# Kernel optimization log

Measured on AMD Instinct MI355X. Metric: run time of the kernel, lower is better.

Reference implementation:

```python
import jax, jax.numpy as jnp
import numpy as np

B, S, D, N = 8, 4096, 1024, 16
EPS = 1e-6


def setup_inputs() -> dict:
    key = jax.random.key(0)
    ks = jax.random.split(key, 6)
    s = 1.0 / np.sqrt(D)
    return {
        "x": jax.random.normal(ks[0], (B, S, D), dtype=jnp.float32),
        "W_lambda": jax.random.uniform(ks[1], (N, D), jnp.float32, -s, s),
        "b_lambda": jnp.full((N,), 2.0, dtype=jnp.float32),  # nn.init.constant_(bias, 2.0)
        "W_B": jax.random.uniform(ks[2], (N, D), jnp.float32, -s, s),
        "W_C": jax.random.uniform(ks[3], (D, N), jnp.float32, -1.0 / np.sqrt(N), 1.0 / np.sqrt(N)),
        "W_gate": jax.random.uniform(ks[4], (D, D), jnp.float32, -s, s),
        "rms_weight": jnp.ones((D,), dtype=jnp.float32),
    }


def reference(x, W_lambda, b_lambda, W_B, W_C, W_gate, rms_weight):
    # Input-dependent decay and input projection, computed for all timesteps at once
    lam = jax.nn.sigmoid(jnp.einsum("bsd,nd->bsn", x, W_lambda) + b_lambda)  # (B,S,N)
    Bx = jnp.einsum("bsd,nd->bsn", x, W_B)  # (B,S,N)

    def step(h, inp):
        l_t, b_t = inp
        h = l_t * h + b_t  # h_t = lambda_t * h_{t-1} + B_t x_t
        return h, h

    h0 = jnp.zeros((x.shape[0], W_B.shape[0]), dtype=x.dtype)
    _, hs = jax.lax.scan(step, h0, (jnp.swapaxes(lam, 0, 1), jnp.swapaxes(Bx, 0, 1)))
    hs = jnp.swapaxes(hs, 0, 1)  # (B,S,N)

    y = jnp.einsum("bsn,dn->bsd", hs, W_C)  # C @ h_t
    gate = jax.nn.sigmoid(jnp.einsum("bsd,ed->bse", x, W_gate))
    y = gate * y
    # RMSNorm
    rms = jax.lax.rsqrt(jnp.mean(y * y, axis=-1, keepdims=True) + EPS)
    return y * rms * rms_weight
```

## Files before the change

kernel.cpp:

```cpp
#include <hip/hip_runtime.h>

#define DD 1024
#define NN 16
#define SS 4096
#define BBATCH 8
#define TOK (BBATCH*SS)

typedef __attribute__((ext_vector_type(8))) __bf16 bf16x8;
typedef __attribute__((ext_vector_type(4))) __bf16 bf16x4;
typedef __attribute__((ext_vector_type(4))) float f32x4;
typedef unsigned int u32;
typedef unsigned long long u64;

__device__ __forceinline__ void async16(void* lds, const void* g) {
  __builtin_amdgcn_global_load_lds(
      (const __attribute__((address_space(1))) u32*)(u64)(g),
      (__attribute__((address_space(3))) u32*)(u32)(u64)(lds), 16, 0, 0);
}

__device__ __forceinline__ float sigmoidf_(float v) {
  return 1.f / (1.f + __expf(-v));
}

__global__ void k_cvtw(const float* __restrict__ wgf, const float* __restrict__ wlf,
                       const float* __restrict__ wbf, __bf16* __restrict__ wg,
                       __bf16* __restrict__ wp) {
  int i = blockIdx.x * blockDim.x + threadIdx.x;
  const int NG = DD * DD / 8, NP = NN * DD / 8;
  const float* src; __bf16* dst;
  if (i < NG)           { src = wgf + (u64)i * 8;            dst = wg + (u64)i * 8; }
  else if (i < NG + NP) { int j = i - NG; src = wlf + j * 8; dst = wp + j * 8; }
  else if (i < NG + 2 * NP) { int j = i - NG - NP; src = wbf + j * 8; dst = wp + NN * DD + j * 8; }
  else return;
  float4 a = *(const float4*)src, b = *(const float4*)(src + 4);
  bf16x8 o;
  o[0] = (__bf16)a.x; o[1] = (__bf16)a.y; o[2] = (__bf16)a.z; o[3] = (__bf16)a.w;
  o[4] = (__bf16)b.x; o[5] = (__bf16)b.y; o[6] = (__bf16)b.z; o[7] = (__bf16)b.w;
  *(bf16x8*)dst = o;
}

__global__ __launch_bounds__(256)
void k_proj(const float* __restrict__ x, const __bf16* __restrict__ wp,
            const float* __restrict__ b_lambda, __bf16* __restrict__ xb,
            float* __restrict__ lam, float* __restrict__ bx) {
  __shared__ __align__(16) __bf16 sA[128 * 32];
  __shared__ __align__(16) __bf16 sB[32 * 32];
  int tid = threadIdx.x;
  int lane = tid & 63, w = tid >> 6;
  int tok0 = blockIdx.x * 128;
  int crow = tid >> 1, cs = (tid & 1) * 2;
  const float* xsrc = x + (u64)(tok0 + crow) * DD + (tid & 1) * 16;
  __bf16* xdst = xb + (u64)(tok0 + crow) * DD + (tid & 1) * 16;
  int sw = (crow & 3) ^ ((crow >> 2) & 3);
  u64 bSrc;
  {
    int u = tid;
    int row = u >> 2, slot = (u & 3) ^ (row & 3);
    bSrc = (u64)((const char*)wp + ((u64)row * DD + slot * 8) * 2);
  }
  f32x4 acc[2][2] = {};
  int r15 = lane & 15, kg = lane >> 4;
  for (int kt = 0; kt < DD / 32; ++kt) {
    float4 a0 = *(const float4*)(xsrc + kt * 32 + 0);
    float4 a1 = *(const float4*)(xsrc + kt * 32 + 4);
    float4 a2 = *(const float4*)(xsrc + kt * 32 + 8);
    float4 a3 = *(const float4*)(xsrc + kt * 32 + 12);
    bf16x8 lo, hi;
    lo[0] = (__bf16)a0.x; lo[1] = (__bf16)a0.y; lo[2] = (__bf16)a0.z; lo[3] = (__bf16)a0.w;
    lo[4] = (__bf16)a1.x; lo[5] = (__bf16)a1.y; lo[6] = (__bf16)a1.z; lo[7] = (__bf16)a1.w;
    hi[0] = (__bf16)a2.x; hi[1] = (__bf16)a2.y; hi[2] = (__bf16)a2.z; hi[3] = (__bf16)a2.w;
    hi[4] = (__bf16)a3.x; hi[5] = (__bf16)a3.y; hi[6] = (__bf16)a3.z; hi[7] = (__bf16)a3.w;
    *(bf16x8*)(xdst + kt * 32) = lo;
    *(bf16x8*)(xdst + kt * 32 + 8) = hi;
    *(bf16x8*)((char*)sA + crow * 64 + ((cs ^ sw) << 4)) = lo;
    *(bf16x8*)((char*)sA + crow * 64 + (((cs + 1) ^ sw) << 4)) = hi;
    if (tid < 128)
      async16((char*)sB + w * 1024, (const void*)(bSrc + kt * 64));
    __syncthreads();
    bf16x8 bfr[2];
#pragma unroll
    for (int nt = 0; nt < 2; ++nt) {
      int brow = nt * 16 + r15;
      bfr[nt] = *(const bf16x8*)((const char*)sB + brow * 64 + ((kg ^ (brow & 3)) << 4));
    }
#pragma unroll
    for (int mt = 0; mt < 2; ++mt) {
      int arow = w * 32 + mt * 16 + r15;
      bf16x8 af = *(const bf16x8*)((const char*)sA + arow * 64 +
                                   ((kg ^ (arow & 3) ^ ((arow >> 2) & 3)) << 4));
#pragma unroll
      for (int nt = 0; nt < 2; ++nt)
        acc[mt][nt] = __builtin_amdgcn_mfma_f32_16x16x32_bf16(af, bfr[nt], acc[mt][nt], 0, 0, 0);
    }
    __syncthreads();
  }
#pragma unroll
  for (int mt = 0; mt < 2; ++mt)
#pragma unroll
    for (int nt = 0; nt < 2; ++nt)
#pragma unroll
      for (int r = 0; r < 4; ++r) {
        int token = tok0 + w * 32 + mt * 16 + kg * 4 + r;
        int j = nt * 16 + r15;
        float v = acc[mt][nt][r];
        if (j < 16) lam[token * NN + j] = sigmoidf_(v + b_lambda[j]);
        else        bx[token * NN + (j - 16)] = v;
      }
}

__global__ __launch_bounds__(256)
void k_scan(const float* __restrict__ lam, const float* __restrict__ bx,
            float* __restrict__ hs) {
  int b = blockIdx.x >> 4, n = blockIdx.x & 15;
  int t = threadIdx.x;
  const int CH = SS / 256;
  float lv[CH], bv[CH];
  int base = (b * SS + t * CH) * NN + n;
  float a = 1.f, bacc = 0.f;
#pragma unroll
  for (int i = 0; i < CH; ++i) {
    lv[i] = lam[base + i * NN];
    bv[i] = bx[base + i * NN];
    bacc = lv[i] * bacc + bv[i];
    a *= lv[i];
  }
  __shared__ float As[2][256], Bs[2][256];
  As[0][t] = a; Bs[0][t] = bacc;
  __syncthreads();
  int cur = 0;
  for (int off = 1; off < 256; off <<= 1) {
    float a2 = As[cur][t], b2 = Bs[cur][t];
    if (t >= off) {
      float ap = As[cur][t - off], bp = Bs[cur][t - off];
      b2 = b2 + a2 * bp;
      a2 = a2 * ap;
    }
    As[cur ^ 1][t] = a2; Bs[cur ^ 1][t] = b2;
    cur ^= 1;
    __syncthreads();
  }
  float h = (t == 0) ? 0.f : Bs[cur][t - 1];
#pragma unroll
  for (int i = 0; i < CH; ++i) {
    h = lv[i] * h + bv[i];
    hs[base + i * NN] = h;
  }
}

#define STG(kt, bi) do { u32 lb = (u32)(bi) * 32768u; u64 ko = (u64)(kt) * 64u;          \
    async16(smc + lb + (u32)w * 1024u,              (const void*)(aAddr0 + ko));         \
    async16(smc + lb + (u32)(8 + w) * 1024u,        (const void*)(aAddr1 + ko));         \
    async16(smc + lb + 16384u + (u32)w * 1024u,     (const void*)(bAddr0 + ko));         \
    async16(smc + lb + 16384u + (u32)(8 + w) * 1024u,(const void*)(bAddr1 + ko)); } while (0)

template<int YB16>
__global__ __launch_bounds__(512, 2)
void k_gemm(const __bf16* __restrict__ xb, const __bf16* __restrict__ wg,
            const float* __restrict__ hs, const float* __restrict__ wc,
            float* __restrict__ outf, __bf16* __restrict__ outb) {
  __shared__ __align__(16) char smc[131072];
  const int tid = threadIdx.x, lane = tid & 63, w = tid >> 6;
  const int r15 = lane & 15, kg = lane >> 4;
  const int wr = w >> 2, wcq = w & 3;
  int bid = blockIdx.x;
  int swz = (bid & 7) * 64 + (bid >> 3);
  int m = swz >> 2, n = swz & 3;
  const int tok0 = m * 256, n0 = n * 256;
  const int sslot = (lane & 3) ^ ((lane >> 2) & 3) ^ ((lane >> 4) & 3);
  const int rA0 = w * 16 + (lane >> 2);
  const int rA1 = (8 + w) * 16 + (lane >> 2);
  const u64 aAddr0 = (u64)(const char*)xb + (u64)(tok0 + rA0) * 2048 + (u32)sslot * 16;
  const u64 aAddr1 = (u64)(const char*)xb + (u64)(tok0 + rA1) * 2048 + (u32)sslot * 16;
  const u64 bAddr0 = (u64)(const char*)wg + (u64)(n0 + rA0) * 2048 + (u32)sslot * 16;
  const u64 bAddr1 = (u64)(const char*)wg + (u64)(n0 + rA1) * 2048 + (u32)sslot * 16;

  f32x4 acc[8][4] = {};

  STG(0, 0); STG(1, 1); STG(2, 2);
  asm volatile("s_waitcnt vmcnt(8)" ::: "memory");
  __builtin_amdgcn_s_barrier();
  __builtin_amdgcn_sched_barrier(0);

  for (int t = 0; t < 32; ++t) {
    if (t + 3 < 32) STG(t + 3, (t + 3) & 3);
    const char* Ab = smc + (t & 3) * 32768;
    const char* Bb = Ab + 16384;
    bf16x8 af[8];
#pragma unroll
    for (int mt = 0; mt < 8; ++mt) {
      int row = wr * 128 + mt * 16 + r15;
      int sl = kg ^ (row & 3) ^ ((row >> 2) & 3);
      af[mt] = *(const bf16x8*)(Ab + row * 64 + sl * 16);
    }
    __builtin_amdgcn_s_setprio(1);
#pragma unroll
    for (int nt = 0; nt < 4; ++nt) {
      int brow = wcq * 64 + nt * 16 + r15;
      int sl = kg ^ (brow & 3) ^ ((brow >> 2) & 3);
      bf16x8 bfr = *(const bf16x8*)(Bb + brow * 64 + sl * 16);
#pragma unroll
      for (int mt = 0; mt < 8; ++mt)
        acc[mt][nt] = __builtin_amdgcn_mfma_f32_16x16x32_bf16(af[mt], bfr, acc[mt][nt], 0, 0, 0);
    }
    __builtin_amdgcn_s_setprio(0);
    if (t < 29)       asm volatile("s_waitcnt vmcnt(8)" ::: "memory");
    else if (t == 29) asm volatile("s_waitcnt vmcnt(4)" ::: "memory");
    else              asm volatile("s_waitcnt vmcnt(0)" ::: "memory");
    __builtin_amdgcn_s_barrier();
    __builtin_amdgcn_sched_barrier(0);
  }

  float* hsl = (float*)smc;
  float* wcl = (float*)(smc + 20480);
  for (int idx = tid; idx < 256 * 16; idx += 512) {
    int r = idx >> 4, c = idx & 15;
    hsl[r * 20 + c] = hs[(u64)tok0 * NN + idx];
    wcl[r * 20 + c] = wc[(u64)n0 * NN + idx];
  }
  __syncthreads();
  f32x4 wcv[4][4];
#pragma unroll
  for (int nt = 0; nt < 4; ++nt) {
    int j = wcq * 64 + nt * 16 + r15;
#pragma unroll
    for (int q = 0; q < 4; ++q) wcv[nt][q] = *(const f32x4*)(wcl + j * 20 + q * 4);
  }
#pragma unroll
  for (int mt = 0; mt < 8; ++mt)
#pragma unroll
    for (int r = 0; r < 4; ++r) {
      int i = wr * 128 + mt * 16 + kg * 4 + r;
      f32x4 hv[4];
#pragma unroll
      for (int q = 0; q < 4; ++q) hv[q] = *(const f32x4*)(hsl + i * 20 + q * 4);
#pragma unroll
      for (int nt = 0; nt < 4; ++nt) {
        f32x4 cv = hv[0] * wcv[nt][0];
        cv += hv[1] * wcv[nt][1];
        cv += hv[2] * wcv[nt][2];
        cv += hv[3] * wcv[nt][3];
        float cy = cv[0] + cv[1] + cv[2] + cv[3];
        float g = sigmoidf_(acc[mt][nt][r]);
        int j = wcq * 64 + nt * 16 + r15;
        u64 off = (u64)(tok0 + i) * DD + n0 + j;
        if (YB16) outb[off] = (__bf16)(g * cy);
        else      outf[off] = g * cy;
      }
    }
}

__global__ __launch_bounds__(256)
void k_norm_b(const __bf16* __restrict__ yb, float* __restrict__ out,
              const float* __restrict__ rw) {
  int row = blockIdx.x * 4 + (threadIdx.x >> 6);
  int lane = threadIdx.x & 63;
  const __bf16* yrow = yb + (u64)row * DD;
  bf16x4 v[4];
  float f[16];
  float rs = 0.f;
#pragma unroll
  for (int q = 0; q < 4; ++q) {
    v[q] = *(const bf16x4*)(yrow + q * 256 + lane * 4);
#pragma unroll
    for (int e = 0; e < 4; ++e) {
      f[q * 4 + e] = (float)v[q][e];
      rs += f[q * 4 + e] * f[q * 4 + e];
    }
  }
#pragma unroll
  for (int msk = 1; msk < 64; msk <<= 1) rs += __shfl_xor(rs, msk, 64);
  float rstd = rsqrtf(rs * (1.f / DD) + 1e-6f);
  float* orow = out + (u64)row * DD;
#pragma unroll
  for (int q = 0; q < 4; ++q) {
    float4 wv = *(const float4*)(rw + q * 256 + lane * 4);
    float4 o;
    o.x = f[q * 4 + 0] * rstd * wv.x;
    o.y = f[q * 4 + 1] * rstd * wv.y;
    o.z = f[q * 4 + 2] * rstd * wv.z;
    o.w = f[q * 4 + 3] * rstd * wv.w;
    *(float4*)(orow + q * 256 + lane * 4) = o;
  }
}

__global__ __launch_bounds__(256)
void k_norm_f(float* __restrict__ out, const float* __restrict__ rw) {
  int row = blockIdx.x * 4 + (threadIdx.x >> 6);
  int lane = threadIdx.x & 63;
  float4* p = (float4*)(out + (u64)row * DD);
  float4 v[4];
  float rs = 0.f;
#pragma unroll
  for (int e = 0; e < 4; ++e) {
    v[e] = p[e * 64 + lane];
    rs += v[e].x * v[e].x + v[e].y * v[e].y + v[e].z * v[e].z + v[e].w * v[e].w;
  }
#pragma unroll
  for (int msk = 1; msk < 64; msk <<= 1) rs += __shfl_xor(rs, msk, 64);
  float rstd = rsqrtf(rs * (1.f / DD) + 1e-6f);
  const float4* rwp = (const float4*)rw;
#pragma unroll
  for (int e = 0; e < 4; ++e) {
    float4 wv = rwp[e * 64 + lane];
    float4 o;
    o.x = v[e].x * rstd * wv.x;
    o.y = v[e].y * rstd * wv.y;
    o.z = v[e].z * rstd * wv.z;
    o.w = v[e].w * rstd * wv.w;
    p[e * 64 + lane] = o;
  }
}

extern "C" void kernel_launch(void* const* d_in, const int* in_sizes, int n_in,
                              void* d_out, int out_size, void* d_ws, size_t ws_size,
                              hipStream_t stream) {
  (void)in_sizes; (void)n_in; (void)out_size;
  const float* x        = (const float*)d_in[0];
  const float* W_lambda = (const float*)d_in[1];
  const float* b_lambda = (const float*)d_in[2];
  const float* W_B      = (const float*)d_in[3];
  const float* W_C      = (const float*)d_in[4];
  const float* W_gate   = (const float*)d_in[5];
  const float* rms_w    = (const float*)d_in[6];
  char* ws = (char*)d_ws;
  __bf16* xb  = (__bf16*)(ws + 0);
  __bf16* wg  = (__bf16*)(ws + 67108864);
  __bf16* wp  = (__bf16*)(ws + 69206016);
  float*  lam = (float*)(ws + 69271552);
  float*  bx  = (float*)(ws + 71368704);
  float*  hs  = (float*)(ws + 73465856);
  __bf16* yb  = (__bf16*)(ws + 75563008);
  float*  out = (float*)d_out;
  bool yb16 = ws_size >= (size_t)(75563008ull + 67108864ull);

  k_cvtw<<<(DD * DD / 8 + 2 * NN * DD / 8 + 255) / 256, 256, 0, stream>>>(
      W_gate, W_lambda, W_B, wg, wp);
  k_proj<<<TOK / 128, 256, 0, stream>>>(x, wp, b_lambda, xb, lam, bx);
  k_scan<<<BBATCH * NN, 256, 0, stream>>>(lam, bx, hs);
  if (yb16) {
    k_gemm<1><<<(TOK / 256) * (DD / 256), 512, 0, stream>>>(xb, wg, hs, W_C, nullptr, yb);
    k_norm_b<<<TOK / 4, 256, 0, stream>>>(yb, out, rms_w);
  } else {
    k_gemm<0><<<(TOK / 256) * (DD / 256), 512, 0, stream>>>(xb, wg, hs, W_C, out, nullptr);
    k_norm_f<<<TOK / 4, 256, 0, stream>>>(out, rms_w);
  }
}
```

Measured before the change: 206.2 us.

## Restructure gate GEMM mainloop into 8-phase ping-pong with K=64 tiles

Replaces the 4-deep ring of K=32 tiles with a double-buffered scheme of K=64 tiles, each split into A/B halves of 128 rows. The loads for future tiles are interleaved between four MFMA phases, each fenced by barriers, and the LDS swizzle is changed to an 8-slot XOR pattern. The aim is to overlap global-to-LDS copies and LDS reads with MFMA work more finely and to halve the number of loop iterations. In exchange it adds many more barriers per iteration and depends on hand-tuned vmcnt and lgkmcnt waits being correct.

```diff
diff --git a/kernel.cpp b/kernel.cpp
--- a/kernel.cpp
+++ b/kernel.cpp
@@ -147,11 +147,12 @@
   }
 }
 
-#define STG(kt, bi) do { u32 lb = (u32)(bi) * 32768u; u64 ko = (u64)(kt) * 64u;          \
-    async16(smc + lb + (u32)w * 1024u,              (const void*)(aAddr0 + ko));         \
-    async16(smc + lb + (u32)(8 + w) * 1024u,        (const void*)(aAddr1 + ko));         \
-    async16(smc + lb + 16384u + (u32)w * 1024u,     (const void*)(bAddr0 + ko));         \
-    async16(smc + lb + 16384u + (u32)(8 + w) * 1024u,(const void*)(bAddr1 + ko)); } while (0)
+#define STAGE(tile, M, h) do {                                                    \
+    u32 lds0 = (u32)(((((tile) & 1) * 4 + (M) * 2 + (h)) << 14) + tid * 16);      \
+    u64 g0 = ((M) ? bBase : aBase) + ((u64)(h) << 18) + (u64)(tile) * 128;        \
+    async16(smc + lds0, (const void*)g0);                                         \
+    async16(smc + lds0 + 8192, (const void*)(g0 + 131072));                       \
+  } while (0)
 
 template<int YB16>
 __global__ __launch_bounds__(512, 2)
@@ -166,49 +167,111 @@
   int swz = (bid & 7) * 64 + (bid >> 3);
   int m = swz >> 2, n = swz & 3;
   const int tok0 = m * 256, n0 = n * 256;
-  const int sslot = (lane & 3) ^ ((lane >> 2) & 3) ^ ((lane >> 4) & 3);
-  const int rA0 = w * 16 + (lane >> 2);
-  const int rA1 = (8 + w) * 16 + (lane >> 2);
-  const u64 aAddr0 = (u64)(const char*)xb + (u64)(tok0 + rA0) * 2048 + (u32)sslot * 16;
-  const u64 aAddr1 = (u64)(const char*)xb + (u64)(tok0 + rA1) * 2048 + (u32)sslot * 16;
-  const u64 bAddr0 = (u64)(const char*)wg + (u64)(n0 + rA0) * 2048 + (u32)sslot * 16;
-  const u64 bAddr1 = (u64)(const char*)wg + (u64)(n0 + rA1) * 2048 + (u32)sslot * 16;
+  const int sslot = (tid & 7) ^ ((tid >> 3) & 7);
+  const u64 aBase = (u64)(const char*)xb + (u64)(tok0 + (tid >> 3)) * 2048 + (u32)sslot * 16;
+  const u64 bBase = (u64)(const char*)wg + (u64)(n0 + (tid >> 3)) * 2048 + (u32)sslot * 16;
+  const u32 sxa0 = (u32)(((0 | kg) ^ (r15 & 7)) * 16);
+  const u32 sxa1 = (u32)(((4 | kg) ^ (r15 & 7)) * 16);
+  const u32 lrB0 = (u32)((wcq & 1) * 64);
 
   f32x4 acc[8][4] = {};
 
-  STG(0, 0); STG(1, 1); STG(2, 2);
-  asm volatile("s_waitcnt vmcnt(8)" ::: "memory");
+  STAGE(0, 0, 0); STAGE(0, 0, 1); STAGE(0, 1, 0); STAGE(0, 1, 1);
+  STAGE(1, 1, 0); STAGE(1, 1, 1); STAGE(1, 0, 0);
+  asm volatile("s_waitcnt vmcnt(6)" ::: "memory");
   __builtin_amdgcn_s_barrier();
-  __builtin_amdgcn_sched_barrier(0);
-
-  for (int t = 0; t < 32; ++t) {
-    if (t + 3 < 32) STG(t + 3, (t + 3) & 3);
-    const char* Ab = smc + (t & 3) * 32768;
-    const char* Bb = Ab + 16384;
-    bf16x8 af[8];
-#pragma unroll
-    for (int mt = 0; mt < 8; ++mt) {
-      int row = wr * 128 + mt * 16 + r15;
-      int sl = kg ^ (row & 3) ^ ((row >> 2) & 3);
-      af[mt] = *(const bf16x8*)(Ab + row * 64 + sl * 16);
-    }
+  asm volatile("" ::: "memory");
+
+  for (int k = 0; k < 16; ++k) {
+    const int b = k & 1;
+    const char* Ah = smc + (u32)((b * 4 + wr) << 14);
+    const char* Bh = smc + (u32)((b * 4 + 2 + (wcq >> 1)) << 14);
+    bf16x8 af[8][2], bfr[4][2];
+#pragma unroll
+    for (int mt = 0; mt < 2; ++mt) {
+      u32 ro = (u32)(mt * 16 + r15) * 128;
+      af[mt][0] = *(const bf16x8*)(Ah + ro + sxa0);
+      af[mt][1] = *(const bf16x8*)(Ah + ro + sxa1);
+    }
+#pragma unroll
+    for (int nt = 0; nt < 4; ++nt) {
+      u32 ro = (lrB0 + (u32)(nt * 16 + r15)) * 128;
+      bfr[nt][0] = *(const bf16x8*)(Bh + ro + sxa0);
+      bfr[nt][1] = *(const bf16x8*)(Bh + ro + sxa1);
+    }
+    if (k <= 14) STAGE(k + 1, 0, 1);
+    __builtin_amdgcn_s_barrier();
+    asm volatile("s_waitcnt lgkmcnt(0)" ::: "memory");
+    __builtin_amdgcn_sched_barrier(0);
     __builtin_amdgcn_s_setprio(1);
 #pragma unroll
-    for (int nt = 0; nt < 4; ++nt) {
-      int brow = wcq * 64 + nt * 16 + r15;
-      int sl = kg ^ (brow & 3) ^ ((brow >> 2) & 3);
-      bf16x8 bfr = *(const bf16x8*)(Bb + brow * 64 + sl * 16);
-#pragma unroll
-      for (int mt = 0; mt < 8; ++mt)
-        acc[mt][nt] = __builtin_amdgcn_mfma_f32_16x16x32_bf16(af[mt], bfr, acc[mt][nt], 0, 0, 0);
-    }
+    for (int mt = 0; mt < 2; ++mt)
+#pragma unroll
+      for (int nt = 0; nt < 4; ++nt) {
+        acc[mt][nt] = __builtin_amdgcn_mfma_f32_16x16x32_bf16(af[mt][0], bfr[nt][0], acc[mt][nt], 0, 0, 0);
+        acc[mt][nt] = __builtin_amdgcn_mfma_f32_16x16x32_bf16(af[mt][1], bfr[nt][1], acc[mt][nt], 0, 0, 0);
+      }
     __builtin_amdgcn_s_setprio(0);
-    if (t < 29)       asm volatile("s_waitcnt vmcnt(8)" ::: "memory");
-    else if (t == 29) asm volatile("s_waitcnt vmcnt(4)" ::: "memory");
-    else              asm volatile("s_waitcnt vmcnt(0)" ::: "memory");
-    __builtin_amdgcn_s_barrier();
+    __builtin_amdgcn_s_barrier();
+    asm volatile("" ::: "memory");
+#pragma unroll
+    for (int mt = 2; mt < 6; ++mt) {
+      u32 ro = (u32)(mt * 16 + r15) * 128;
+      af[mt][0] = *(const bf16x8*)(Ah + ro + sxa0);
+      af[mt][1] = *(const bf16x8*)(Ah + ro + sxa1);
+    }
+    if (k <= 13) STAGE(k + 2, 1, 0);
+    __builtin_amdgcn_s_barrier();
+    asm volatile("s_waitcnt lgkmcnt(0)" ::: "memory");
     __builtin_amdgcn_sched_barrier(0);
-  }
+    __builtin_amdgcn_s_setprio(1);
+#pragma unroll
+    for (int mt = 2; mt < 4; ++mt)
+#pragma unroll
+      for (int nt = 0; nt < 4; ++nt) {
+        acc[mt][nt] = __builtin_amdgcn_mfma_f32_16x16x32_bf16(af[mt][0], bfr[nt][0], acc[mt][nt], 0, 0, 0);
+        acc[mt][nt] = __builtin_amdgcn_mfma_f32_16x16x32_bf16(af[mt][1], bfr[nt][1], acc[mt][nt], 0, 0, 0);
+      }
+    __builtin_amdgcn_s_setprio(0);
+    __builtin_amdgcn_s_barrier();
+    asm volatile("" ::: "memory");
+#pragma unroll
+    for (int mt = 6; mt < 8; ++mt) {
+      u32 ro = (u32)(mt * 16 + r15) * 128;
+      af[mt][0] = *(const bf16x8*)(Ah + ro + sxa0);
+      af[mt][1] = *(const bf16x8*)(Ah + ro + sxa1);
+    }
+    if (k <= 13) STAGE(k + 2, 1, 1);
+    __builtin_amdgcn_s_barrier();
+    asm volatile("s_waitcnt lgkmcnt(0)" ::: "memory");
+    __builtin_amdgcn_sched_barrier(0);
+    __builtin_amdgcn_s_setprio(1);
+#pragma unroll
+    for (int mt = 4; mt < 6; ++mt)
+#pragma unroll
+      for (int nt = 0; nt < 4; ++nt) {
+        acc[mt][nt] = __builtin_amdgcn_mfma_f32_16x16x32_bf16(af[mt][0], bfr[nt][0], acc[mt][nt], 0, 0, 0);
+        acc[mt][nt] = __builtin_amdgcn_mfma_f32_16x16x32_bf16(af[mt][1], bfr[nt][1], acc[mt][nt], 0, 0, 0);
+      }
+    __builtin_amdgcn_s_setprio(0);
+    __builtin_amdgcn_s_barrier();
+    asm volatile("" ::: "memory");
+    if (k <= 13) STAGE(k + 2, 0, 0);
+    if (k <= 13)      asm volatile("s_waitcnt vmcnt(6)" ::: "memory");
+    else if (k == 14) asm volatile("s_waitcnt vmcnt(0)" ::: "memory");
+    __builtin_amdgcn_s_barrier();
+    asm volatile("" ::: "memory");
+    __builtin_amdgcn_s_setprio(1);
+#pragma unroll
+    for (int mt = 6; mt < 8; ++mt)
+#pragma unroll
+      for (int nt = 0; nt < 4; ++nt) {
+        acc[mt][nt] = __builtin_amdgcn_mfma_f32_16x16x32_bf16(af[mt][0], bfr[nt][0], acc[mt][nt], 0, 0, 0);
+        acc[mt][nt] = __builtin_amdgcn_mfma_f32_16x16x32_bf16(af[mt][1], bfr[nt][1], acc[mt][nt], 0, 0, 0);
+      }
+    __builtin_amdgcn_s_setprio(0);
+  }
+  asm volatile("" ::: "memory");
 
   float* hsl = (float*)smc;
   float* wcl = (float*)(smc + 20480);
```

New measurement: 199.9 us. -3.1%, faster.
